# Kernel tuning notes

Hardware: AMD Instinct MI355X
Metric: run time of the kernel (lower is better)

Reference implementation:

```python
import jax, jax.numpy as jnp
import numpy as np

B, S, D, H, DK, DV = 2, 2048, 1024, 16, 64, 64


def setup_inputs() -> dict:
    key = jax.random.key(0)
    ks = jax.random.split(key, 12)
    s = 0.02
    return {
        "q": jax.random.normal(ks[0], (B, S, D), jnp.float32),
        "k": jax.random.normal(ks[1], (B, S, D), jnp.float32),
        "v": jax.random.normal(ks[2], (B, S, D), jnp.float32),
        "attn_mask": jax.random.bernoulli(ks[3], 0.1, (B, S, S)),
        "wq": jax.random.normal(ks[4], (D, H * DK), jnp.float32) * s,
        "bq": jnp.zeros((H * DK,), jnp.float32),
        "wk": jax.random.normal(ks[5], (D, H * DK), jnp.float32) * s,
        "bk": jnp.zeros((H * DK,), jnp.float32),
        "wv": jax.random.normal(ks[6], (D, H * DV), jnp.float32) * s,
        "bv": jnp.zeros((H * DV,), jnp.float32),
        "wo": jax.random.normal(ks[7], (H * DV, D), jnp.float32) * s,
        "bo": jnp.zeros((D,), jnp.float32),
        "gamma": jnp.ones((D,), jnp.float32),
        "beta": jnp.zeros((D,), jnp.float32),
    }


def reference(q, k, v, attn_mask, wq, bq, wk, bk, wv, bv, wo, bo, gamma, beta):
    residual = q
    # projections -> [B, H, S, dk/dv]
    qh = (q @ wq + bq).reshape(B, S, H, DK).transpose(0, 2, 1, 3)
    kh = (k @ wk + bk).reshape(B, S, H, DK).transpose(0, 2, 1, 3)
    vh = (v @ wv + bv).reshape(B, S, H, DV).transpose(0, 2, 1, 3)
    scores = jnp.einsum("bhqd,bhkd->bhqk", qh, kh) / np.sqrt(DK).astype(np.float32)
    scores = jnp.where(attn_mask[:, None, :, :], jnp.float32(-1e9), scores)
    attn = jax.nn.softmax(scores, axis=-1)
    context = jnp.einsum("bhqk,bhkd->bhqd", attn, vh)
    context = context.transpose(0, 2, 1, 3).reshape(B, S, H * DV)
    out = context @ wo + bo + residual
    # LayerNorm (eps=1e-5, torch default)
    mu = out.mean(-1, keepdims=True)
    var = out.var(-1, keepdims=True)
    out = (out - mu) * jax.lax.rsqrt(var + 1e-5) * gamma + beta
    return out, attn
```

## Files before the change

### kernel.cpp

```cpp
#include <hip/hip_runtime.h>
#include <hip/hip_bf16.h>

#define BB 2
#define SS 2048
#define DD 1024
#define HH 16
#define DKV 64

typedef __attribute__((ext_vector_type(8))) short short8;
typedef __attribute__((ext_vector_type(4))) short short4_t;
typedef __attribute__((ext_vector_type(4))) float f32x4;

#define MFMA16(a, b, c) __builtin_amdgcn_mfma_f32_16x16x32_bf16(a, b, c, 0, 0, 0)

__device__ __forceinline__ short f2bf(float f) {
    __hip_bfloat16 h = __float2bfloat16(f);
    union { __hip_bfloat16 h; short s; } u;
    u.h = h;
    return u.s;
}

__global__ __launch_bounds__(256) void wtrans_kernel(
    const float* __restrict__ w0, const float* __restrict__ w1,
    const float* __restrict__ w2, const float* __restrict__ w3,
    short* __restrict__ o0, short* __restrict__ o1,
    short* __restrict__ o2, short* __restrict__ o3)
{
    const int z = blockIdx.z;
    const float* W = (z == 0) ? w0 : (z == 1) ? w1 : (z == 2) ? w2 : w3;
    short* O = (z == 0) ? o0 : (z == 1) ? o1 : (z == 2) ? o2 : o3;
    __shared__ short T[64][72];
    const int t = threadIdx.x;
    const int k0 = blockIdx.x * 64, n0 = blockIdx.y * 64;
    const int row = t >> 2, c = (t & 3) * 16;
    const float* src = W + (size_t)(k0 + row) * DD + n0 + c;
    #pragma unroll
    for (int i = 0; i < 16; i += 4) {
        float4 f = *(const float4*)(src + i);
        T[c + i + 0][row] = f2bf(f.x);
        T[c + i + 1][row] = f2bf(f.y);
        T[c + i + 2][row] = f2bf(f.z);
        T[c + i + 3][row] = f2bf(f.w);
    }
    __syncthreads();
    const int nr = t >> 2, kc = (t & 3) * 16;
    *(short8*)(O + (size_t)(n0 + nr) * DD + k0 + kc)     = *(const short8*)&T[nr][kc];
    *(short8*)(O + (size_t)(n0 + nr) * DD + k0 + kc + 8) = *(const short8*)&T[nr][kc + 8];
}

__global__ __launch_bounds__(256) void proj3_kernel(
    const float* __restrict__ A0, const float* __restrict__ A1, const float* __restrict__ A2,
    const short* __restrict__ WT0, const short* __restrict__ WT1, const short* __restrict__ WT2,
    const float* __restrict__ bq, const float* __restrict__ bk, const float* __restrict__ bv,
    __hip_bfloat16* __restrict__ o0, __hip_bfloat16* __restrict__ o1, __hip_bfloat16* __restrict__ o2,
    const int* __restrict__ mask, unsigned long long* __restrict__ bits)
{
    const int t = threadIdx.x;
    const int lane = t & 63;
    const int wave = t >> 6;

    if (blockIdx.z == 0) {
        const int bid = blockIdx.y * 32 + blockIdx.x;
        const int base = bid * 512 + wave * 128;
        #pragma unroll 4
        for (int wi = base; wi < base + 128; ++wi) {
            const int mv = mask[(size_t)wi * 64 + lane];
            const unsigned long long bal = __ballot(mv != 0);
            if (lane == 0) bits[wi] = bal;
        }
        return;
    }

    const int z = blockIdx.z - 1;
    const float* A  = (z == 0) ? A0 : (z == 1) ? A1 : A2;
    const short* WT = (z == 0) ? WT0 : (z == 1) ? WT1 : WT2;
    const float* bias = (z == 0) ? bq : (z == 1) ? bk : bv;
    __hip_bfloat16* outh = (z == 0) ? o0 : (z == 1) ? o1 : o2;

    __shared__ __align__(16) short As[128][40];
    __shared__ __align__(16) short Bs[128][40];
    const int wm = wave >> 1, wn = wave & 1;
    const int m0 = blockIdx.x * 128, n0 = blockIdx.y * 128;
    const int lr = lane & 15;
    const int kb = (lane >> 4) * 8;
    const int row2 = t >> 1, kk2 = (t & 1) * 16;

    f32x4 acc[4][4] = {};

    for (int k0 = 0; k0 < DD; k0 += 32) {
        __syncthreads();
        {
            const float* src = A + (size_t)(m0 + row2) * DD + k0 + kk2;
            float4 fa = *(const float4*)(src);
            float4 fb = *(const float4*)(src + 4);
            float4 fc = *(const float4*)(src + 8);
            float4 fd = *(const float4*)(src + 12);
            short8 v0 = { f2bf(fa.x), f2bf(fa.y), f2bf(fa.z), f2bf(fa.w),
                          f2bf(fb.x), f2bf(fb.y), f2bf(fb.z), f2bf(fb.w) };
            short8 v1 = { f2bf(fc.x), f2bf(fc.y), f2bf(fc.z), f2bf(fc.w),
                          f2bf(fd.x), f2bf(fd.y), f2bf(fd.z), f2bf(fd.w) };
            *(short8*)&As[row2][kk2]     = v0;
            *(short8*)&As[row2][kk2 + 8] = v1;
        }
        {
            const short8* srcw = (const short8*)(WT + (size_t)(n0 + row2) * DD + k0 + kk2);
            *(short8*)&Bs[row2][kk2]     = srcw[0];
            *(short8*)&Bs[row2][kk2 + 8] = srcw[1];
        }
        __syncthreads();
        short8 af[4], bfr[4];
        #pragma unroll
        for (int i = 0; i < 4; i++) af[i]  = *(const short8*)&As[wm * 64 + i * 16 + lr][kb];
        #pragma unroll
        for (int j = 0; j < 4; j++) bfr[j] = *(const short8*)&Bs[wn * 64 + j * 16 + lr][kb];
        #pragma unroll
        for (int i = 0; i < 4; i++)
            #pragma unroll
            for (int j = 0; j < 4; j++)
                acc[i][j] = MFMA16(af[i], bfr[j], acc[i][j]);
    }

    if (z != 2) {
        #pragma unroll
        for (int j = 0; j < 4; j++) {
            const int col = n0 + wn * 64 + j * 16 + lr;
            const float bvv = bias[col];
            const int h = col >> 6, d = col & 63;
            #pragma unroll
            for (int i = 0; i < 4; i++) {
                #pragma unroll
                for (int r = 0; r < 4; r++) {
                    const int m = m0 + wm * 64 + i * 16 + (lane >> 4) * 4 + r;
                    const int b = m >> 11, s = m & (SS - 1);
                    outh[(((size_t)(b * HH + h)) * SS + s) * DKV + d] =
                        __float2bfloat16(acc[i][j][r] + bvv);
                }
            }
        }
    } else {
        short* vT = (short*)outh;
        #pragma unroll
        for (int j = 0; j < 4; j++) {
            const int col = n0 + wn * 64 + j * 16 + lr;
            const float bvv = bias[col];
            const int h = col >> 6, d = col & 63;
            #pragma unroll
            for (int i = 0; i < 4; i++) {
                const int m = m0 + wm * 64 + i * 16 + (lane >> 4) * 4;
                const int b = m >> 11, s = m & (SS - 1);
                short4_t pk;
                #pragma unroll
                for (int r = 0; r < 4; r++) pk[r] = f2bf(acc[i][j][r] + bvv);
                *(short4_t*)(vT + ((size_t)(b * HH + h) * DKV + d) * SS + s) = pk;
            }
        }
    }
}

__global__ __launch_bounds__(256) void outproj_kernel(
    const __hip_bfloat16* __restrict__ Actx, const short* __restrict__ WT,
    const float* __restrict__ bias, const float* __restrict__ resid,
    float* __restrict__ out)
{
    __shared__ __align__(16) short As[128][40];
    __shared__ __align__(16) short Bs[128][40];
    const int t = threadIdx.x;
    const int lane = t & 63;
    const int wave = t >> 6;
    const int wm = wave >> 1, wn = wave & 1;
    const int m0 = blockIdx.x * 128, n0 = blockIdx.y * 128;
    const int lr = lane & 15;
    const int kb = (lane >> 4) * 8;
    const int row2 = t >> 1, kk2 = (t & 1) * 16;

    f32x4 acc[4][4] = {};

    for (int k0 = 0; k0 < DD; k0 += 32) {
        __syncthreads();
        {
            const short8* src = (const short8*)((const short*)Actx + (size_t)(m0 + row2) * DD + k0 + kk2);
            *(short8*)&As[row2][kk2]     = src[0];
            *(short8*)&As[row2][kk2 + 8] = src[1];
        }
        {
            const short8* srcw = (const short8*)(WT + (size_t)(n0 + row2) * DD + k0 + kk2);
            *(short8*)&Bs[row2][kk2]     = srcw[0];
            *(short8*)&Bs[row2][kk2 + 8] = srcw[1];
        }
        __syncthreads();
        short8 af[4], bfr[4];
        #pragma unroll
        for (int i = 0; i < 4; i++) af[i]  = *(const short8*)&As[wm * 64 + i * 16 + lr][kb];
        #pragma unroll
        for (int j = 0; j < 4; j++) bfr[j] = *(const short8*)&Bs[wn * 64 + j * 16 + lr][kb];
        #pragma unroll
        for (int i = 0; i < 4; i++)
            #pragma unroll
            for (int j = 0; j < 4; j++)
                acc[i][j] = MFMA16(af[i], bfr[j], acc[i][j]);
    }

    #pragma unroll
    for (int j = 0; j < 4; j++) {
        const int col = n0 + wn * 64 + j * 16 + lr;
        const float bvv = bias[col];
        #pragma unroll
        for (int i = 0; i < 4; i++) {
            #pragma unroll
            for (int r = 0; r < 4; r++) {
                const int m = m0 + wm * 64 + i * 16 + (lane >> 4) * 4 + r;
                out[(size_t)m * DD + col] = acc[i][j][r] + bvv + resid[(size_t)m * DD + col];
            }
        }
    }
}

__global__ __launch_bounds__(512) void attn_compute_kernel(
    const __hip_bfloat16* __restrict__ qh, const __hip_bfloat16* __restrict__ kh,
    const __hip_bfloat16* __restrict__ vT, const unsigned long long* __restrict__ bits,
    float* __restrict__ linvb, __hip_bfloat16* __restrict__ ctx)
{
    __shared__ __align__(16) short Ks[2][64][72];
    __shared__ __align__(16) short Vs[2][64][72];
    __shared__ __align__(16) short Ps[8][16][72];
    const int t = threadIdx.x, lane = t & 63, w = t >> 6;

    const int logical = (blockIdx.x & 7) * 64 + (blockIdx.x >> 3);
    const int qt = logical & 15;
    const int bh = logical >> 4;
    const int h = bh & (HH - 1);
    const int b = bh >> 4;
    const int q0w = qt * 128 + w * 16;
    const size_t headbase = (size_t)bh * SS * DKV;
    const int lr = lane & 15;
    const int kb = (lane >> 4) * 8;
    const int Q4 = lane >> 4;
    const int rbase = Q4 * 4;

    const short* kbase = (const short*)kh + headbase;
    const short* vbase = (const short*)vT + (size_t)bh * DKV * SS;
    const unsigned long long* bitrow = bits + ((size_t)b * SS + q0w) * (SS / 64);

    const int srow = t >> 3, sc8 = (t & 7) * 8;
    const short* kstg = kbase + (size_t)srow * DKV + sc8;
    const short* vstg = vbase + (size_t)srow * SS + sc8;

    const short* qrp = (const short*)qh + headbase + (size_t)(q0w + lr) * DKV;
    const short8 aq0 = *(const short8*)(qrp + kb);
    const short8 aq1 = *(const short8*)(qrp + 32 + kb);

    float lsum[4] = {0.f, 0.f, 0.f, 0.f};
    f32x4 cacc[4] = {};

    {
        short8 kreg = *(const short8*)(kstg);
        short8 vreg = *(const short8*)(vstg);
        *(short8*)&Ks[0][srow][sc8] = kreg;
        *(short8*)&Vs[0][srow][sc8] = vreg;
        __syncthreads();
        for (int kt = 0; kt < 32; ++kt) {
            const int cur = kt & 1;
            if (kt + 1 < 32) {
                kreg = *(const short8*)(kstg + (size_t)(kt + 1) * 64 * DKV);
                vreg = *(const short8*)(vstg + (size_t)(kt + 1) * 64);
            }
            f32x4 sc[4];
            __builtin_amdgcn_s_setprio(1);
            #pragma unroll
            for (int fc = 0; fc < 4; ++fc) {
                short8 bk0 = *(const short8*)&Ks[cur][fc * 16 + lr][kb];
                short8 bk1 = *(const short8*)&Ks[cur][fc * 16 + lr][32 + kb];
                f32x4 s = {0.f, 0.f, 0.f, 0.f};
                s = MFMA16(aq0, bk0, s);
                s = MFMA16(aq1, bk1, s);
                sc[fc] = s;
            }
            __builtin_amdgcn_s_setprio(0);
            unsigned long long mw[4];
            #pragma unroll
            for (int r = 0; r < 4; ++r)
                mw[r] = bitrow[(size_t)(rbase + r) * (SS / 64) + kt];
            #pragma unroll
            for (int fc = 0; fc < 4; ++fc)
                #pragma unroll
                for (int r = 0; r < 4; ++r) {
                    const bool masked = (mw[r] >> (fc * 16 + lr)) & 1ull;
                    const float p = masked ? 0.f : __expf(sc[fc][r] * 0.125f);
                    lsum[r] += p;
                    Ps[w][rbase + r][fc * 16 + lr] = f2bf(p);
                }
            short8 ap0 = *(const short8*)&Ps[w][lr][kb];
            short8 ap1 = *(const short8*)&Ps[w][lr][32 + kb];
            __builtin_amdgcn_s_setprio(1);
            #pragma unroll
            for (int fd = 0; fd < 4; ++fd) {
                short8 bv0 = *(const short8*)&Vs[cur][fd * 16 + lr][kb];
                short8 bv1 = *(const short8*)&Vs[cur][fd * 16 + lr][32 + kb];
                cacc[fd] = MFMA16(ap0, bv0, cacc[fd]);
                cacc[fd] = MFMA16(ap1, bv1, cacc[fd]);
            }
            __builtin_amdgcn_s_setprio(0);
            if (kt + 1 < 32) {
                *(short8*)&Ks[cur ^ 1][srow][sc8] = kreg;
                *(short8*)&Vs[cur ^ 1][srow][sc8] = vreg;
            }
            __syncthreads();
        }
    }
    #pragma unroll
    for (int r = 0; r < 4; r++) {
        float s = lsum[r];
        s += __shfl_xor(s, 1);
        s += __shfl_xor(s, 2);
        s += __shfl_xor(s, 4);
        s += __shfl_xor(s, 8);
        lsum[r] = s;
    }
    float linv[4];
    #pragma unroll
    for (int r = 0; r < 4; r++) linv[r] = 1.f / lsum[r];

    if (lr == 0) {
        #pragma unroll
        for (int r = 0; r < 4; r++)
            linvb[(size_t)bh * SS + q0w + rbase + r] = linv[r];
    }

    #pragma unroll
    for (int fd = 0; fd < 4; ++fd)
        #pragma unroll
        for (int r = 0; r < 4; r++) {
            const int qrow = q0w + rbase + r;
            ctx[((size_t)b * SS + qrow) * DD + h * DKV + fd * 16 + lr] =
                __float2bfloat16(cacc[fd][r] * linv[r]);
        }
}

__global__ __launch_bounds__(256) void attn_store_kernel(
    const __hip_bfloat16* __restrict__ qh, const __hip_bfloat16* __restrict__ kh,
    const unsigned long long* __restrict__ bits, const float* __restrict__ linvb,
    float* __restrict__ attn)
{
    __shared__ __align__(16) short Ks[512][72];
    const int t = threadIdx.x, lane = t & 63, w = t >> 6;
    const int qt = blockIdx.x;
    const int kc = blockIdx.y;
    const int bh = blockIdx.z;
    const int b = bh >> 4;
    const int q0w = qt * 64 + w * 16;
    const int k0c = kc * 512;
    const size_t headbase = (size_t)bh * SS * DKV;
    const int lr = lane & 15;
    const int kb = (lane >> 4) * 8;
    const int Q4 = lane >> 4;
    const int rbase = Q4 * 4;

    {
        const short* kbase = (const short*)kh + headbase + (size_t)k0c * DKV;
        const int c8 = (t & 7) * 8;
        #pragma unroll
        for (int sweep = 0; sweep < 16; ++sweep) {
            const int row = (t >> 3) + sweep * 32;
            *(short8*)&Ks[row][c8] = *(const short8*)(kbase + (size_t)row * DKV + c8);
        }
    }

    const short* qrp = (const short*)qh + headbase + (size_t)(q0w + lr) * DKV;
    const short8 aq0 = *(const short8*)(qrp + kb);
    const short8 aq1 = *(const short8*)(qrp + 32 + kb);

    float linv[4];
    #pragma unroll
    for (int r = 0; r < 4; ++r)
        linv[r] = linvb[(size_t)bh * SS + q0w + rbase + r];

    const unsigned long long* bitrow = bits + ((size_t)b * SS + q0w) * (SS / 64);
    float* arow = attn + ((size_t)bh * SS + q0w) * SS + k0c;

    __syncthreads();

    for (int g = 0; g < 8; ++g) {
        unsigned long long mw[4];
        #pragma unroll
        for (int r = 0; r < 4; ++r)
            mw[r] = bitrow[(size_t)(rbase + r) * (SS / 64) + kc * 8 + g];
        #pragma unroll
        for (int fc = 0; fc < 4; ++fc) {
            const int col = g * 64 + fc * 16;
            short8 bk0 = *(const short8*)&Ks[col + lr][kb];
            short8 bk1 = *(const short8*)&Ks[col + lr][32 + kb];
            f32x4 s = {0.f, 0.f, 0.f, 0.f};
            s = MFMA16(aq0, bk0, s);
            s = MFMA16(aq1, bk1, s);
            #pragma unroll
            for (int r = 0; r < 4; ++r) {
                const bool masked = (mw[r] >> (fc * 16 + lr)) & 1ull;
                const float p = masked ? 0.f : __expf(s[r] * 0.125f) * linv[r];
                arow[(size_t)(rbase + r) * SS + col + lr] = p;
            }
        }
    }
}

__global__ __launch_bounds__(256) void ln_kernel(
    float* __restrict__ io, const float* __restrict__ g, const float* __restrict__ bta)
{
    const int row = blockIdx.x;
    const int t = threadIdx.x;
    float* p = io + (size_t)row * DD;
    float4 x = *(float4*)(p + t * 4);
    float s  = x.x + x.y + x.z + x.w;
    float s2 = x.x * x.x + x.y * x.y + x.z * x.z + x.w * x.w;
    #pragma unroll
    for (int off = 32; off; off >>= 1) {
        s  += __shfl_xor(s, off);
        s2 += __shfl_xor(s2, off);
    }
    __shared__ float as_[4], bs_[4];
    const int w = t >> 6, l = t & 63;
    if (!l) { as_[w] = s; bs_[w] = s2; }
    __syncthreads();
    s  = as_[0] + as_[1] + as_[2] + as_[3];
    s2 = bs_[0] + bs_[1] + bs_[2] + bs_[3];
    const float mu  = s * (1.f / DD);
    const float var = s2 * (1.f / DD) - mu * mu;
    const float rs  = rsqrtf(var + 1e-5f);
    float4 gv = *(const float4*)(g + t * 4);
    float4 bv = *(const float4*)(bta + t * 4);
    float4 o;
    o.x = (x.x - mu) * rs * gv.x + bv.x;
    o.y = (x.y - mu) * rs * gv.y + bv.y;
    o.z = (x.z - mu) * rs * gv.z + bv.z;
    o.w = (x.w - mu) * rs * gv.w + bv.w;
    *(float4*)(p + t * 4) = o;
}

extern "C" void kernel_launch(void* const* d_in, const int* in_sizes, int n_in,
                              void* d_out, int out_size, void* d_ws, size_t ws_size,
                              hipStream_t stream)
{
    (void)in_sizes; (void)n_in; (void)out_size; (void)ws_size;
    const float* q     = (const float*)d_in[0];
    const float* k     = (const float*)d_in[1];
    const float* v     = (const float*)d_in[2];
    const int*   mask  = (const int*)d_in[3];
    const float* wq    = (const float*)d_in[4];
    const float* bq    = (const float*)d_in[5];
    const float* wk    = (const float*)d_in[6];
    const float* bk    = (const float*)d_in[7];
    const float* wv    = (const float*)d_in[8];
    const float* bv    = (const float*)d_in[9];
    const float* wo    = (const float*)d_in[10];
    const float* bo    = (const float*)d_in[11];
    const float* gamma = (const float*)d_in[12];
    const float* beta  = (const float*)d_in[13];

    float* out  = (float*)d_out;
    float* attn = out + (size_t)BB * SS * DD;

    const size_t hsz = (size_t)BB * HH * SS * DKV;
    __hip_bfloat16* qhp = (__hip_bfloat16*)d_ws;
    __hip_bfloat16* khp = qhp + hsz;
    __hip_bfloat16* vTp = khp + hsz;
    __hip_bfloat16* ctx = vTp + hsz;
    unsigned long long* bits = (unsigned long long*)(ctx + hsz);
    float* linvb = (float*)(bits + (size_t)BB * SS * (SS / 64));
    short* wtq = (short*)(linvb + (size_t)BB * HH * SS);
    short* wtk = wtq + (size_t)DD * DD;
    short* wtv = wtk + (size_t)DD * DD;
    short* wto = wtv + (size_t)DD * DD;

    dim3 gw(16, 16, 4);
    wtrans_kernel<<<gw, 256, 0, stream>>>(wq, wk, wv, wo, wtq, wtk, wtv, wto);

    dim3 gg(32, 8, 4);
    proj3_kernel<<<gg, 256, 0, stream>>>(q, k, v, wtq, wtk, wtv, bq, bk, bv,
                                         qhp, khp, vTp, mask, bits);
    attn_compute_kernel<<<BB * HH * 16, 512, 0, stream>>>(qhp, khp, vTp, bits, linvb, ctx);
    dim3 gs(32, 4, BB * HH);
    attn_store_kernel<<<gs, 256, 0, stream>>>(qhp, khp, bits, linvb, attn);
    dim3 go(32, 8);
    outproj_kernel<<<go, 256, 0, stream>>>(ctx, wto, bo, q, out);
    ln_kernel<<<BB * SS, 256, 0, stream>>>(out, gamma, beta);
}
```

Measured before the change: 369.8 us.

## Pre-convert q/k/v to bf16 and merge out-projection with attention-store kernel

Adds q/k/v fp32-to-bf16 conversion blocks to the weight-transpose kernel so the projection GEMM loads bf16 directly instead of converting fp32 on every K-tile. The out-projection GEMM and the attention-probability store kernel are merged into one launch, distinguished by blockIdx.z, so the small outproj grid runs concurrently with the bandwidth-heavy attn store. This trades extra workspace writes/reads for the bf16 copies and a larger shared LDS allocation per block.

```diff
diff --git a/kernel.cpp b/kernel.cpp
--- a/kernel.cpp
+++ b/kernel.cpp
@@ -23,14 +23,30 @@
 __global__ __launch_bounds__(256) void wtrans_kernel(
     const float* __restrict__ w0, const float* __restrict__ w1,
     const float* __restrict__ w2, const float* __restrict__ w3,
+    const float* __restrict__ qf, const float* __restrict__ kf, const float* __restrict__ vf,
     short* __restrict__ o0, short* __restrict__ o1,
-    short* __restrict__ o2, short* __restrict__ o3)
+    short* __restrict__ o2, short* __restrict__ o3,
+    short* __restrict__ oq, short* __restrict__ ok, short* __restrict__ ov)
 {
     const int z = blockIdx.z;
+    const int t = threadIdx.x;
+    if (z >= 4) {
+        const float* src = (z == 4) ? qf : (z == 5) ? kf : vf;
+        short* dst = (z == 4) ? oq : (z == 5) ? ok : ov;
+        size_t idx = ((size_t)(blockIdx.y * 16 + blockIdx.x) * 256 + t) * 8;
+        #pragma unroll
+        for (int it = 0; it < 8; ++it, idx += 524288) {
+            float4 a = *(const float4*)(src + idx);
+            float4 b = *(const float4*)(src + idx + 4);
+            short8 p = { f2bf(a.x), f2bf(a.y), f2bf(a.z), f2bf(a.w),
+                         f2bf(b.x), f2bf(b.y), f2bf(b.z), f2bf(b.w) };
+            *(short8*)(dst + idx) = p;
+        }
+        return;
+    }
     const float* W = (z == 0) ? w0 : (z == 1) ? w1 : (z == 2) ? w2 : w3;
     short* O = (z == 0) ? o0 : (z == 1) ? o1 : (z == 2) ? o2 : o3;
     __shared__ short T[64][72];
-    const int t = threadIdx.x;
     const int k0 = blockIdx.x * 64, n0 = blockIdx.y * 64;
     const int row = t >> 2, c = (t & 3) * 16;
     const float* src = W + (size_t)(k0 + row) * DD + n0 + c;
@@ -49,7 +65,7 @@
 }
 
 __global__ __launch_bounds__(256) void proj3_kernel(
-    const float* __restrict__ A0, const float* __restrict__ A1, const float* __restrict__ A2,
+    const short* __restrict__ A0, const short* __restrict__ A1, const short* __restrict__ A2,
     const short* __restrict__ WT0, const short* __restrict__ WT1, const short* __restrict__ WT2,
     const float* __restrict__ bq, const float* __restrict__ bk, const float* __restrict__ bv,
     __hip_bfloat16* __restrict__ o0, __hip_bfloat16* __restrict__ o1, __hip_bfloat16* __restrict__ o2,
@@ -72,7 +88,7 @@
     }
 
     const int z = blockIdx.z - 1;
-    const float* A  = (z == 0) ? A0 : (z == 1) ? A1 : A2;
+    const short* A  = (z == 0) ? A0 : (z == 1) ? A1 : A2;
     const short* WT = (z == 0) ? WT0 : (z == 1) ? WT1 : WT2;
     const float* bias = (z == 0) ? bq : (z == 1) ? bk : bv;
     __hip_bfloat16* outh = (z == 0) ? o0 : (z == 1) ? o1 : o2;
@@ -90,17 +106,9 @@
     for (int k0 = 0; k0 < DD; k0 += 32) {
         __syncthreads();
         {
-            const float* src = A + (size_t)(m0 + row2) * DD + k0 + kk2;
-            float4 fa = *(const float4*)(src);
-            float4 fb = *(const float4*)(src + 4);
-            float4 fc = *(const float4*)(src + 8);
-            float4 fd = *(const float4*)(src + 12);
-            short8 v0 = { f2bf(fa.x), f2bf(fa.y), f2bf(fa.z), f2bf(fa.w),
-                          f2bf(fb.x), f2bf(fb.y), f2bf(fb.z), f2bf(fb.w) };
-            short8 v1 = { f2bf(fc.x), f2bf(fc.y), f2bf(fc.z), f2bf(fc.w),
-                          f2bf(fd.x), f2bf(fd.y), f2bf(fd.z), f2bf(fd.w) };
-            *(short8*)&As[row2][kk2]     = v0;
-            *(short8*)&As[row2][kk2 + 8] = v1;
+            const short8* srca = (const short8*)(A + (size_t)(m0 + row2) * DD + k0 + kk2);
+            *(short8*)&As[row2][kk2]     = srca[0];
+            *(short8*)&As[row2][kk2 + 8] = srca[1];
         }
         {
             const short8* srcw = (const short8*)(WT + (size_t)(n0 + row2) * DD + k0 + kk2);
@@ -152,64 +160,6 @@
                 #pragma unroll
                 for (int r = 0; r < 4; r++) pk[r] = f2bf(acc[i][j][r] + bvv);
                 *(short4_t*)(vT + ((size_t)(b * HH + h) * DKV + d) * SS + s) = pk;
-            }
-        }
-    }
-}
-
-__global__ __launch_bounds__(256) void outproj_kernel(
-    const __hip_bfloat16* __restrict__ Actx, const short* __restrict__ WT,
-    const float* __restrict__ bias, const float* __restrict__ resid,
-    float* __restrict__ out)
-{
-    __shared__ __align__(16) short As[128][40];
-    __shared__ __align__(16) short Bs[128][40];
-    const int t = threadIdx.x;
-    const int lane = t & 63;
-    const int wave = t >> 6;
-    const int wm = wave >> 1, wn = wave & 1;
-    const int m0 = blockIdx.x * 128, n0 = blockIdx.y * 128;
-    const int lr = lane & 15;
-    const int kb = (lane >> 4) * 8;
-    const int row2 = t >> 1, kk2 = (t & 1) * 16;
-
-    f32x4 acc[4][4] = {};
-
-    for (int k0 = 0; k0 < DD; k0 += 32) {
-        __syncthreads();
-        {
-            const short8* src = (const short8*)((const short*)Actx + (size_t)(m0 + row2) * DD + k0 + kk2);
-            *(short8*)&As[row2][kk2]     = src[0];
-            *(short8*)&As[row2][kk2 + 8] = src[1];
-        }
-        {
-            const short8* srcw = (const short8*)(WT + (size_t)(n0 + row2) * DD + k0 + kk2);
-            *(short8*)&Bs[row2][kk2]     = srcw[0];
-            *(short8*)&Bs[row2][kk2 + 8] = srcw[1];
-        }
-        __syncthreads();
-        short8 af[4], bfr[4];
-        #pragma unroll
-        for (int i = 0; i < 4; i++) af[i]  = *(const short8*)&As[wm * 64 + i * 16 + lr][kb];
-        #pragma unroll
-        for (int j = 0; j < 4; j++) bfr[j] = *(const short8*)&Bs[wn * 64 + j * 16 + lr][kb];
-        #pragma unroll
-        for (int i = 0; i < 4; i++)
-            #pragma unroll
-            for (int j = 0; j < 4; j++)
-                acc[i][j] = MFMA16(af[i], bfr[j], acc[i][j]);
-    }
-
-    #pragma unroll
-    for (int j = 0; j < 4; j++) {
-        const int col = n0 + wn * 64 + j * 16 + lr;
-        const float bvv = bias[col];
-        #pragma unroll
-        for (int i = 0; i < 4; i++) {
-            #pragma unroll
-            for (int r = 0; r < 4; r++) {
-                const int m = m0 + wm * 64 + i * 16 + (lane >> 4) * 4 + r;
-                out[(size_t)m * DD + col] = acc[i][j][r] + bvv + resid[(size_t)m * DD + col];
             }
         }
     }
@@ -336,22 +286,79 @@
         }
 }
 
-__global__ __launch_bounds__(256) void attn_store_kernel(
+__global__ __launch_bounds__(256) void outstore_kernel(
+    const __hip_bfloat16* __restrict__ Actx, const short* __restrict__ WT,
+    const float* __restrict__ bias, const float* __restrict__ resid,
+    float* __restrict__ out,
     const __hip_bfloat16* __restrict__ qh, const __hip_bfloat16* __restrict__ kh,
     const unsigned long long* __restrict__ bits, const float* __restrict__ linvb,
     float* __restrict__ attn)
 {
-    __shared__ __align__(16) short Ks[512][72];
+    __shared__ __align__(16) short LDSBUF[36864];
     const int t = threadIdx.x, lane = t & 63, w = t >> 6;
-    const int qt = blockIdx.x;
-    const int kc = blockIdx.y;
-    const int bh = blockIdx.z;
+    const int lr = lane & 15;
+    const int kb = (lane >> 4) * 8;
+
+    if (blockIdx.z == 0) {
+        short (*As)[40] = (short(*)[40])LDSBUF;
+        short (*Bs)[40] = (short(*)[40])(LDSBUF + 5120);
+        const int wave = w;
+        const int wm = wave >> 1, wn = wave & 1;
+        const int m0 = blockIdx.x * 128, n0 = blockIdx.y * 128;
+        const int row2 = t >> 1, kk2 = (t & 1) * 16;
+
+        f32x4 acc[4][4] = {};
+
+        for (int k0 = 0; k0 < DD; k0 += 32) {
+            __syncthreads();
+            {
+                const short8* src = (const short8*)((const short*)Actx + (size_t)(m0 + row2) * DD + k0 + kk2);
+                *(short8*)&As[row2][kk2]     = src[0];
+                *(short8*)&As[row2][kk2 + 8] = src[1];
+            }
+            {
+                const short8* srcw = (const short8*)(WT + (size_t)(n0 + row2) * DD + k0 + kk2);
+                *(short8*)&Bs[row2][kk2]     = srcw[0];
+                *(short8*)&Bs[row2][kk2 + 8] = srcw[1];
+            }
+            __syncthreads();
+            short8 af[4], bfr[4];
+            #pragma unroll
+            for (int i = 0; i < 4; i++) af[i]  = *(const short8*)&As[wm * 64 + i * 16 + lr][kb];
+            #pragma unroll
+            for (int j = 0; j < 4; j++) bfr[j] = *(const short8*)&Bs[wn * 64 + j * 16 + lr][kb];
+            #pragma unroll
+            for (int i = 0; i < 4; i++)
+                #pragma unroll
+                for (int j = 0; j < 4; j++)
+                    acc[i][j] = MFMA16(af[i], bfr[j], acc[i][j]);
+        }
+
+        #pragma unroll
+        for (int j = 0; j < 4; j++) {
+            const int col = n0 + wn * 64 + j * 16 + lr;
+            const float bvv = bias[col];
+            #pragma unroll
+            for (int i = 0; i < 4; i++) {
+                #pragma unroll
+                for (int r = 0; r < 4; r++) {
+                    const int m = m0 + wm * 64 + i * 16 + (lane >> 4) * 4 + r;
+                    out[(size_t)m * DD + col] = acc[i][j][r] + bvv + resid[(size_t)m * DD + col];
+                }
+            }
+        }
+        return;
+    }
+
+    short (*Ks)[72] = (short(*)[72])LDSBUF;
+    const int sb = (blockIdx.z - 1) * 256 + blockIdx.y * 32 + blockIdx.x;
+    const int qt = sb & 31;
+    const int kc = (sb >> 5) & 3;
+    const int bh = sb >> 7;
     const int b = bh >> 4;
     const int q0w = qt * 64 + w * 16;
     const int k0c = kc * 512;
     const size_t headbase = (size_t)bh * SS * DKV;
-    const int lr = lane & 15;
-    const int kb = (lane >> 4) * 8;
     const int Q4 = lane >> 4;
     const int rbase = Q4 * 4;
 
@@ -469,17 +476,21 @@
     short* wtk = wtq + (size_t)DD * DD;
     short* wtv = wtk + (size_t)DD * DD;
     short* wto = wtv + (size_t)DD * DD;
-
-    dim3 gw(16, 16, 4);
-    wtrans_kernel<<<gw, 256, 0, stream>>>(wq, wk, wv, wo, wtq, wtk, wtv, wto);
+    short* qb  = wto + (size_t)DD * DD;
+    short* kb2 = qb  + (size_t)BB * SS * DD;
+    short* vb2 = kb2 + (size_t)BB * SS * DD;
+
+    dim3 gw(16, 16, 7);
+    wtrans_kernel<<<gw, 256, 0, stream>>>(wq, wk, wv, wo, q, k, v,
+                                          wtq, wtk, wtv, wto, qb, kb2, vb2);
 
     dim3 gg(32, 8, 4);
-    proj3_kernel<<<gg, 256, 0, stream>>>(q, k, v, wtq, wtk, wtv, bq, bk, bv,
+    proj3_kernel<<<gg, 256, 0, stream>>>(qb, kb2, vb2, wtq, wtk, wtv, bq, bk, bv,
                                          qhp, khp, vTp, mask, bits);
     attn_compute_kernel<<<BB * HH * 16, 512, 0, stream>>>(qhp, khp, vTp, bits, linvb, ctx);
-    dim3 gs(32, 4, BB * HH);
-    attn_store_kernel<<<gs, 256, 0, stream>>>(qhp, khp, bits, linvb, attn);
-    dim3 go(32, 8);
-    outproj_kernel<<<go, 256, 0, stream>>>(ctx, wto, bo, q, out);
+
+    dim3 gm(32, 8, 17);
+    outstore_kernel<<<gm, 256, 0, stream>>>(ctx, wto, bo, q, out,
+                                            qhp, khp, bits, linvb, attn);
     ln_kernel<<<BB * SS, 256, 0, stream>>>(out, gamma, beta);
 }
```

Result: faster. 330.3 us (-10.7%).
